# Kernel optimization log

Measured on AMD Instinct MI355X. Metric: run time of the kernel, lower is better.

## Reference

```python
import jax, jax.numpy as jnp
import numpy as np
import math

B, T, C = 2, 2048, 1024
NH = 16
HD = C // NH

def setup_inputs() -> dict:
    key = jax.random.key(0)
    ks = jax.random.split(key, 3)
    scale = 0.02
    return {
        "x": jax.random.normal(ks[0], (B, T, C), dtype=jnp.float32),
        "Wqkv": jax.random.normal(ks[1], (C, 3 * C), dtype=jnp.float32) * scale,
        "bqkv": jnp.zeros((3 * C,), dtype=jnp.float32),
        "Wproj": jax.random.normal(ks[2], (C, C), dtype=jnp.float32) * scale,
        "bproj": jnp.zeros((C,), dtype=jnp.float32),
    }

def reference(x, Wqkv, bqkv, Wproj, bproj):
    b, t, c = x.shape
    qkv = x @ Wqkv + bqkv                      # (B,T,3C)
    qkv = qkv.reshape(b, t, 3, NH, HD)
    q = jnp.transpose(qkv[:, :, 0], (0, 2, 1, 3))  # (B,H,T,D)
    k = jnp.transpose(qkv[:, :, 1], (0, 2, 1, 3))
    v = jnp.transpose(qkv[:, :, 2], (0, 2, 1, 3))
    att = jnp.einsum('bhqd,bhkd->bhqk', q, k) / math.sqrt(HD)
    causal = jnp.tril(jnp.ones((t, t), dtype=bool))
    att = jnp.where(causal[None, None], att, jnp.float32(-jnp.inf))
    att = jax.nn.softmax(att, axis=-1)
    y = jnp.einsum('bhqk,bhkd->bhqd', att, v)  # (B,H,T,D)
    y = jnp.transpose(y, (0, 2, 1, 3)).reshape(b, t, c)
    return y @ Wproj + bproj
```

## Files before the change

kernel.cpp:

```cpp
#include <hip/hip_runtime.h>


typedef __attribute__((ext_vector_type(8))) short short8;
typedef __attribute__((ext_vector_type(4))) short short4v;
typedef __attribute__((ext_vector_type(4))) float f32x4;
typedef __attribute__((ext_vector_type(2))) unsigned int u32x2;
struct ushort4_t { unsigned short x, y, z, w; };

#define MFMA16(a, b, c) __builtin_amdgcn_mfma_f32_16x16x32_bf16((a), (b), (c), 0, 0, 0)
#define MFMA16K16(a, b, c) __builtin_amdgcn_mfma_f32_16x16x16bf16_1k((a), (b), (c), 0, 0, 0)

__device__ __forceinline__ unsigned short f2bf(float f) {
  unsigned u = __builtin_bit_cast(unsigned, f);
  u += 0x7fffu + ((u >> 16) & 1u);
  return (unsigned short)(u >> 16);
}

__device__ __forceinline__ unsigned short f2bf_fast(float f) {
  return (unsigned short)((__builtin_bit_cast(unsigned, f) + 0x8000u) >> 16);
}

#if __has_builtin(__builtin_amdgcn_cvt_pk_bf16_f32)
typedef __attribute__((ext_vector_type(2))) __bf16 bf16x2;
__device__ __forceinline__ short4v pack_bf16x4(float a, float b, float c, float d) {
  bf16x2 lo = __builtin_amdgcn_cvt_pk_bf16_f32(a, b);
  bf16x2 hi = __builtin_amdgcn_cvt_pk_bf16_f32(c, d);
  u32x2 t;
  t[0] = __builtin_bit_cast(unsigned, lo);
  t[1] = __builtin_bit_cast(unsigned, hi);
  return __builtin_bit_cast(short4v, t);
}
#else
__device__ __forceinline__ short4v pack_bf16x4(float a, float b, float c, float d) {
  short4v r;
  r[0] = (short)f2bf_fast(a); r[1] = (short)f2bf_fast(b);
  r[2] = (short)f2bf_fast(c); r[3] = (short)f2bf_fast(d);
  return r;
}
#endif

__device__ __forceinline__ void gl2lds16(const void* g, void* l) {
  __builtin_amdgcn_global_load_lds(
      (__attribute__((address_space(1))) void*)g,
      (__attribute__((address_space(3))) void*)l,
      16, 0, 0);
}

__global__ __launch_bounds__(256) void conv_bf16(const float* __restrict__ src,
                                                 unsigned short* __restrict__ dst,
                                                 int n) {
  int i = (blockIdx.x * 256 + threadIdx.x) * 4;
  if (i >= n) return;
  float4 f = *(const float4*)(src + i);
  unsigned long long r = (unsigned long long)f2bf(f.x)
      | ((unsigned long long)f2bf(f.y) << 16)
      | ((unsigned long long)f2bf(f.z) << 32)
      | ((unsigned long long)f2bf(f.w) << 48);
  *(unsigned long long*)(dst + i) = r;
}

__global__ __launch_bounds__(256) void transpose_conv(const float* __restrict__ W,
                                                      unsigned short* __restrict__ WT,
                                                      int K, int N) {
  __shared__ float tile[64][65];
  const int n0 = blockIdx.x * 64, k0 = blockIdx.y * 64;
  const int tid = threadIdx.x;
  const int c = tid & 63, rbase = tid >> 6;
#pragma unroll
  for (int i = 0; i < 16; ++i) {
    int r = i * 4 + rbase;
    tile[r][c] = W[(size_t)(k0 + r) * N + n0 + c];
  }
  __syncthreads();
#pragma unroll
  for (int i = 0; i < 16; ++i) {
    int r = i * 4 + rbase;
    WT[(size_t)(n0 + r) * K + k0 + c] = f2bf(tile[c][r]);
  }
}

template <int EPI, int MT>
__global__ __launch_bounds__(256)
void gemm_bt(const unsigned short* __restrict__ A,
             const unsigned short* __restrict__ BT,
             const float* __restrict__ bias,
             float* __restrict__ outF,
             unsigned short* __restrict__ q_out,
             unsigned short* __restrict__ k_out,
             unsigned short* __restrict__ vT_out,
             int Ndim, int Kdim) {
  constexpr int IF = MT / 32;
  constexpr int RA = MT / 32;
  __shared__ __align__(16) unsigned short As[MT * 64];
  __shared__ __align__(16) unsigned short Bs[128 * 64];
  const int tid = threadIdx.x;
  const int wave = tid >> 6, lane = tid & 63;
  const int quad = lane >> 4, lr = lane & 15;
  const int wm = wave >> 1, wn = wave & 1;
  const int m0 = blockIdx.y * MT, n0 = blockIdx.x * 128;

  const int r_l = tid >> 3;
  const int cg = (tid & 7) ^ (r_l & 7);
  const unsigned short* gA = A + (size_t)(m0 + r_l) * Kdim + cg * 8;
  const unsigned short* gB = BT + (size_t)(n0 + r_l) * Kdim + cg * 8;
  const size_t rstep = (size_t)32 * Kdim;

  f32x4 acc[IF][4] = {};
  for (int k0 = 0; k0 < Kdim; k0 += 64) {
#pragma unroll
    for (int rd = 0; rd < RA; ++rd)
      gl2lds16(gA + k0 + rd * rstep, As + rd * 2048 + wave * 512);
#pragma unroll
    for (int rd = 0; rd < 4; ++rd)
      gl2lds16(gB + k0 + rd * rstep, Bs + rd * 2048 + wave * 512);
    __syncthreads();
#pragma unroll
    for (int s = 0; s < 2; ++s) {
      const int sw = ((s * 4 + quad) ^ (lr & 7)) * 8;
      short8 a[IF], b[4];
#pragma unroll
      for (int i = 0; i < IF; ++i)
        a[i] = *(const short8*)(As + (wm * (MT / 2) + i * 16 + lr) * 64 + sw);
#pragma unroll
      for (int j = 0; j < 4; ++j)
        b[j] = *(const short8*)(Bs + (wn * 64 + j * 16 + lr) * 64 + sw);
#pragma unroll
      for (int i = 0; i < IF; ++i)
#pragma unroll
        for (int j = 0; j < 4; ++j)
          acc[i][j] = MFMA16(a[i], b[j], acc[i][j]);
    }
    __syncthreads();
  }

  const int row_t = wm * (MT / 2) + quad * 4;
  const int col_t = wn * 64 + lr;
  if (EPI == 0) {
    const int sec = n0 >> 10;
    const float scl = (sec == 0) ? 0.18033688f : 1.0f;
#pragma unroll
    for (int j = 0; j < 4; ++j) {
      const int n = n0 + col_t + j * 16;
      const float bi = bias[n];
      const int nn = n & 1023, h = nn >> 6, d = nn & 63;
#pragma unroll
      for (int i = 0; i < IF; ++i) {
        const int m_base = m0 + row_t + i * 16;
        const int bb = m_base >> 11, t0 = m_base & 2047;
        const int bh = bb * 16 + h;
        if (sec == 2) {
          ushort4_t pk;
          pk.x = f2bf(acc[i][j][0] + bi);
          pk.y = f2bf(acc[i][j][1] + bi);
          pk.z = f2bf(acc[i][j][2] + bi);
          pk.w = f2bf(acc[i][j][3] + bi);
          *(ushort4_t*)(vT_out + ((size_t)bh * 64 + d) * 2048 + t0) = pk;
        } else {
          unsigned short* dst = (sec == 0 ? q_out : k_out) + (size_t)bh * 131072 + t0 * 64 + d;
#pragma unroll
          for (int r = 0; r < 4; ++r)
            dst[r * 64] = f2bf((acc[i][j][r] + bi) * scl);
        }
      }
    }
  } else {
#pragma unroll
    for (int i = 0; i < IF; ++i)
#pragma unroll
      for (int r = 0; r < 4; ++r) {
        const int m = m0 + row_t + i * 16 + r;
#pragma unroll
        for (int j = 0; j < 4; ++j) {
          const int n = n0 + col_t + j * 16;
          outF[(size_t)m * Ndim + n] = acc[i][j][r] + bias[n];
        }
      }
  }
}

__global__ __launch_bounds__(256, 3)
void attn(const unsigned short* __restrict__ qbuf,
          const unsigned short* __restrict__ kbuf,
          const unsigned short* __restrict__ vT,
          unsigned short* __restrict__ yb) {
  __shared__ __align__(16) unsigned short Ks[3][4096];
  __shared__ __align__(16) unsigned short Vs[3][4096];
  const int tid = threadIdx.x, wave = tid >> 6, lane = tid & 63;
  const int quad = lane >> 4, lr = lane & 15;
  const int bh = blockIdx.x;
  const int qt = 31 - (int)blockIdx.y;
  const int qrow0 = qt * 64;

  const unsigned short* qp0 = qbuf + (size_t)bh * 131072;
  const unsigned short* kp0 = kbuf + (size_t)bh * 131072;
  const unsigned short* vp0 = vT   + (size_t)bh * 131072;

  short8 aq[2];
  {
    const unsigned short* qp =
        qp0 + (size_t)(qrow0 + wave * 16 + lr) * 64 + quad * 8;
    aq[0] = *(const short8*)qp;
    aq[1] = *(const short8*)(qp + 32);
  }

  short4v ones4;
#pragma unroll
  for (int i = 0; i < 4; ++i) ones4[i] = (short)0x3F80;

  const int sr = tid >> 3;
  const int scg = (tid & 7) ^ (sr & 7);
  int kbase[2];
#pragma unroll
  for (int h = 0; h < 2; ++h)
    kbase[h] = lr * 64 + (((quad + 4 * h) ^ (lr & 7)) << 3);
  int vbase[4];
#pragma unroll
  for (int kb = 0; kb < 4; ++kb)
    vbase[kb] = lr * 64 + (((2 * kb + (quad >> 1)) ^ (lr & 7)) << 3) + (quad & 1) * 4;

  f32x4 o[4] = {};
  f32x4 lacc = {};

  auto stage = [&](int buf, int kt) {
    const unsigned short* kg = kp0 + (size_t)(kt * 64 + sr) * 64 + scg * 8;
    const unsigned short* vg = vp0 + (size_t)sr * 2048 + kt * 64 + scg * 8;
    gl2lds16(kg,             &Ks[buf][wave * 512]);
    gl2lds16(kg + 32 * 64,   &Ks[buf][2048 + wave * 512]);
    gl2lds16(vg,             &Vs[buf][wave * 512]);
    gl2lds16(vg + 32 * 2048, &Vs[buf][2048 + wave * 512]);
  };

  const int dlast = qt;
  stage(0, 0);
  if (dlast >= 1) stage(1, 1);
  int buf = 0;
  for (int kt = 0; kt <= dlast; ++kt) {
    if (kt < dlast) __builtin_amdgcn_s_waitcnt(0x0F74);
    else            __builtin_amdgcn_s_waitcnt(0x0F70);
    __builtin_amdgcn_s_barrier();
    if (kt + 2 <= dlast) {
      int nb = buf + 2; if (nb >= 3) nb -= 3;
      stage(nb, kt + 2);
    }
    const unsigned short* Kb = Ks[buf];
    const unsigned short* Vb = Vs[buf];
    short8 bk[4][2];
#pragma unroll
    for (int jt = 0; jt < 4; ++jt) {
      bk[jt][0] = *(const short8*)(Kb + jt * 1024 + kbase[0]);
      bk[jt][1] = *(const short8*)(Kb + jt * 1024 + kbase[1]);
    }
    f32x4 s[4] = {};
#pragma unroll
    for (int jt = 0; jt < 4; ++jt) {
      s[jt] = MFMA16(bk[jt][0], aq[0], s[jt]);
      s[jt] = MFMA16(bk[jt][1], aq[1], s[jt]);
    }
    short4v pa[4];
    if (kt == dlast) {
      const int qloc = wave * 16 + lr;
#pragma unroll
      for (int jt = 0; jt < 4; ++jt) {
        float p[4];
#pragma unroll
        for (int r = 0; r < 4; ++r) {
          p[r] = __builtin_amdgcn_exp2f(s[jt][r]);
          if (jt * 16 + quad * 4 + r > qloc) p[r] = 0.f;
        }
        pa[jt] = pack_bf16x4(p[0], p[1], p[2], p[3]);
      }
    } else {
#pragma unroll
      for (int jt = 0; jt < 4; ++jt) {
        float p[4];
#pragma unroll
        for (int r = 0; r < 4; ++r) p[r] = __builtin_amdgcn_exp2f(s[jt][r]);
        pa[jt] = pack_bf16x4(p[0], p[1], p[2], p[3]);
      }
    }
#pragma unroll
    for (int kb = 0; kb < 4; ++kb)
      lacc = MFMA16K16(ones4, pa[kb], lacc);
#pragma unroll
    for (int kb = 0; kb < 4; ++kb)
#pragma unroll
      for (int jd = 0; jd < 4; ++jd) {
        const short4v bv = *(const short4v*)(Vb + jd * 1024 + vbase[kb]);
        o[jd] = MFMA16K16(pa[kb], bv, o[jd]);
      }
    buf += 1; if (buf >= 3) buf -= 3;
  }

  const int b = bh >> 4, h = bh & 15;
  float inv[4];
#pragma unroll
  for (int r = 0; r < 4; ++r)
    inv[r] = __builtin_amdgcn_rcpf(__shfl(lacc[0], quad * 4 + r));
#pragma unroll
  for (int jd = 0; jd < 4; ++jd)
#pragma unroll
    for (int r = 0; r < 4; ++r) {
      const int t = qrow0 + wave * 16 + quad * 4 + r;
      yb[((size_t)b * 2048 + t) * 1024 + h * 64 + jd * 16 + lr] =
          f2bf(o[jd][r] * inv[r]);
    }
}

extern "C" void kernel_launch(void* const* d_in, const int* in_sizes, int n_in,
                              void* d_out, int out_size, void* d_ws, size_t ws_size,
                              hipStream_t stream) {
  const float* x     = (const float*)d_in[0];
  const float* Wqkv  = (const float*)d_in[1];
  const float* bqkv  = (const float*)d_in[2];
  const float* Wproj = (const float*)d_in[3];
  const float* bproj = (const float*)d_in[4];
  float* out = (float*)d_out;

  char* ws = (char*)d_ws;
  unsigned short* xb     = (unsigned short*)(ws);
  unsigned short* wqkvT  = (unsigned short*)(ws + 8388608);
  unsigned short* wprojT = (unsigned short*)(ws + 14680064);
  unsigned short* qbuf   = (unsigned short*)(ws + 16777216);
  unsigned short* kbuf   = (unsigned short*)(ws + 25165824);
  unsigned short* vTbuf  = (unsigned short*)(ws + 33554432);
  unsigned short* ybuf   = (unsigned short*)(ws + 41943040);

  conv_bf16<<<4096, 256, 0, stream>>>(x, xb, 4194304);
  transpose_conv<<<dim3(48, 16), 256, 0, stream>>>(Wqkv, wqkvT, 1024, 3072);
  transpose_conv<<<dim3(16, 16), 256, 0, stream>>>(Wproj, wprojT, 1024, 1024);
  gemm_bt<0, 128><<<dim3(24, 32), 256, 0, stream>>>(xb, wqkvT, bqkv, nullptr,
                                                    qbuf, kbuf, vTbuf, 3072, 1024);
  attn<<<dim3(32, 32), 256, 0, stream>>>(qbuf, kbuf, vTbuf, ybuf);
  gemm_bt<1, 64><<<dim3(8, 64), 256, 0, stream>>>(ybuf, wprojT, bproj, out,
                                                  nullptr, nullptr, nullptr, 1024, 1024);
}
```

Measured before the change: 180.7 us.

## Triple-buffer GEMM LDS staging with vmcnt waits and shrink QKV tile

The GEMM mainloop moves from a single LDS buffer with two barriers per k-step to a three-stage ring. Tiles are prefetched two steps ahead, and the only synchronisation is a vmcnt wait that leaves one stage in flight plus a single barrier. This is meant to overlap global-to-LDS loads with MFMA work. Separately, the QKV GEMM uses 64-row tiles, doubling the grid for better CU occupancy, at the cost of more B-tile reloads and triple the LDS footprint.

```diff
diff --git a/kernel.cpp b/kernel.cpp
--- a/kernel.cpp
+++ b/kernel.cpp
@@ -91,8 +91,10 @@
              int Ndim, int Kdim) {
   constexpr int IF = MT / 32;
   constexpr int RA = MT / 32;
-  __shared__ __align__(16) unsigned short As[MT * 64];
-  __shared__ __align__(16) unsigned short Bs[128 * 64];
+  constexpr int NSTG = RA + 4;
+  constexpr int WAIT_KEEP1 = 0x0F70 + NSTG;
+  __shared__ __align__(16) unsigned short As[3][MT * 64];
+  __shared__ __align__(16) unsigned short Bs[3][128 * 64];
   const int tid = threadIdx.x;
   const int wave = tid >> 6, lane = tid & 63;
   const int quad = lane >> 4, lr = lane & 15;
@@ -104,33 +106,48 @@
   const unsigned short* gA = A + (size_t)(m0 + r_l) * Kdim + cg * 8;
   const unsigned short* gB = BT + (size_t)(n0 + r_l) * Kdim + cg * 8;
   const size_t rstep = (size_t)32 * Kdim;
+  const int NT = Kdim >> 6;
+
+  auto stageT = [&](int bufi, int kt) {
+#pragma unroll
+    for (int rd = 0; rd < RA; ++rd)
+      gl2lds16(gA + kt * 64 + rd * rstep, &As[bufi][rd * 2048 + wave * 512]);
+#pragma unroll
+    for (int rd = 0; rd < 4; ++rd)
+      gl2lds16(gB + kt * 64 + rd * rstep, &Bs[bufi][rd * 2048 + wave * 512]);
+  };
 
   f32x4 acc[IF][4] = {};
-  for (int k0 = 0; k0 < Kdim; k0 += 64) {
-#pragma unroll
-    for (int rd = 0; rd < RA; ++rd)
-      gl2lds16(gA + k0 + rd * rstep, As + rd * 2048 + wave * 512);
-#pragma unroll
-    for (int rd = 0; rd < 4; ++rd)
-      gl2lds16(gB + k0 + rd * rstep, Bs + rd * 2048 + wave * 512);
-    __syncthreads();
+  stageT(0, 0);
+  if (NT > 1) stageT(1, 1);
+  int bufc = 0;
+  for (int kt = 0; kt < NT; ++kt) {
+    if (kt < NT - 1) __builtin_amdgcn_s_waitcnt(WAIT_KEEP1);
+    else             __builtin_amdgcn_s_waitcnt(0x0F70);
+    __builtin_amdgcn_s_barrier();
+    if (kt + 2 < NT) {
+      int nb = bufc + 2; if (nb >= 3) nb -= 3;
+      stageT(nb, kt + 2);
+    }
+    const unsigned short* Ab = As[bufc];
+    const unsigned short* Bb = Bs[bufc];
 #pragma unroll
     for (int s = 0; s < 2; ++s) {
       const int sw = ((s * 4 + quad) ^ (lr & 7)) * 8;
       short8 a[IF], b[4];
 #pragma unroll
       for (int i = 0; i < IF; ++i)
-        a[i] = *(const short8*)(As + (wm * (MT / 2) + i * 16 + lr) * 64 + sw);
+        a[i] = *(const short8*)(Ab + (wm * (MT / 2) + i * 16 + lr) * 64 + sw);
 #pragma unroll
       for (int j = 0; j < 4; ++j)
-        b[j] = *(const short8*)(Bs + (wn * 64 + j * 16 + lr) * 64 + sw);
+        b[j] = *(const short8*)(Bb + (wn * 64 + j * 16 + lr) * 64 + sw);
 #pragma unroll
       for (int i = 0; i < IF; ++i)
 #pragma unroll
         for (int j = 0; j < 4; ++j)
           acc[i][j] = MFMA16(a[i], b[j], acc[i][j]);
     }
-    __syncthreads();
+    bufc += 1; if (bufc >= 3) bufc -= 3;
   }
 
   const int row_t = wm * (MT / 2) + quad * 4;
@@ -328,8 +345,8 @@
   conv_bf16<<<4096, 256, 0, stream>>>(x, xb, 4194304);
   transpose_conv<<<dim3(48, 16), 256, 0, stream>>>(Wqkv, wqkvT, 1024, 3072);
   transpose_conv<<<dim3(16, 16), 256, 0, stream>>>(Wproj, wprojT, 1024, 1024);
-  gemm_bt<0, 128><<<dim3(24, 32), 256, 0, stream>>>(xb, wqkvT, bqkv, nullptr,
-                                                    qbuf, kbuf, vTbuf, 3072, 1024);
+  gemm_bt<0, 64><<<dim3(24, 64), 256, 0, stream>>>(xb, wqkvT, bqkv, nullptr,
+                                                   qbuf, kbuf, vTbuf, 3072, 1024);
   attn<<<dim3(32, 32), 256, 0, stream>>>(qbuf, kbuf, vTbuf, ybuf);
   gemm_bt<1, 64><<<dim3(8, 64), 256, 0, stream>>>(ybuf, wprojT, bproj, out,
                                                   nullptr, nullptr, nullptr, 1024, 1024);
```

Result: slower. 188.4 us (+4.3%).
